# Performance work log

Measured on AMD Instinct MI355X. Metric: run time of the kernel, lower is better.

The kernel has to match this reference:

```python
import math
import jax, jax.numpy as jnp
import numpy as np

GRAIN = 300   # bilinear / grain dim (gpconv output channels)
PAD = 4       # explicit zero padding before each conv1d / conv2d
POOL = 40     # adaptive pool target (mf_model_pool_dim)

def conv1d_k2(x, w, b):
    # x: [B, L, Cin], w: [Cout, Cin, 2] -> [B, L-1, Cout]
    return (jnp.einsum('blc,oc->blo', x[:, :-1], w[:, :, 0])
            + jnp.einsum('blc,oc->blo', x[:, 1:], w[:, :, 1]) + b)

def kmax_last(x, k):
    # torch-style k-max pooling: top-k values along last axis, original order kept
    idx = jnp.sort(jax.lax.top_k(x, k)[1], axis=-1)
    return jnp.take_along_axis(x, idx, axis=-1)

def kmax_len(x, k):
    # k-max pooling over the length axis (axis=1) of [B, L, C]
    return jnp.swapaxes(kmax_last(jnp.swapaxes(x, 1, 2), k), 1, 2)

def adaptive_max_1d(x, out, axis):
    # torch AdaptiveMaxPool semantics along one axis; windows precomputed statically
    L = x.shape[axis]
    r = np.arange(out)
    starts = (r * L) // out
    ends = -((-(r + 1) * L) // out)
    maxw = int((ends - starts).max())
    off = starts[:, None] + np.arange(maxw)[None, :]
    mask = jnp.asarray(off < ends[:, None])
    idxs = np.minimum(off, L - 1)
    xm = jnp.moveaxis(x, axis, -1)
    g = jnp.where(mask, xm[..., idxs], -jnp.inf)
    return jnp.moveaxis(g.max(-1), -1, axis)

def conv2d_p4(x, w, b):
    y = jax.lax.conv_general_dilated(x, w, (1, 1), [(PAD, PAD), (PAD, PAD)],
                                     dimension_numbers=('NCHW', 'OIHW', 'NCHW'))
    return y + b[None, :, None, None]

def gp_tower(x, w1, b1, w2, b2, w3, b3, k1, k2):
    # multigranular conv tower: zero-pad(4) -> conv1d(k=2) -> tanh -> k-max pool
    g0 = kmax_last(x, GRAIN)                      # [B, L, 300]
    def block(z, w, b, k):
        z = jnp.pad(z, ((0, 0), (PAD, PAD), (0, 0)))
        return kmax_len(jnp.tanh(conv1d_k2(z, w, b)), k)
    p1 = block(x, w1, b1, k1)                     # [B, k1, 300]
    p2 = block(p1, w2, b2, k2)                    # [B, k2, 300]
    p3 = block(p2, w3, b3, 1)                     # [B, 1, 300]
    return jnp.concatenate([g0, p1, p2, p3], axis=1)

def _forward(query, pos_doc, neg_docs, qw1, qb1, qw2, qb2, qw3, qb3,
             dw1, db1, dw2, db2, dw3, db3, bw, bb,
             mw1, mb1, mw2, mb2, mw3, mb3, lw, lb):
    B, Lq, _ = query.shape
    S, _, Ld, _ = neg_docs.shape
    kq1, kq2 = max(4, math.ceil(2 * Lq / 3)), max(4, math.ceil(Lq / 3))
    kd1, kd2 = max(4, math.ceil(2 * Ld / 3)), max(4, math.ceil(Ld / 3))
    qg = gp_tower(query, qw1, qb1, qw2, qb2, qw3, qb3, kq1, kq2)   # [B, Nq, 300]
    docs = jnp.concatenate([pos_doc[None], neg_docs], 0).reshape((S + 1) * B, Ld, -1)
    dg = gp_tower(docs, dw1, db1, dw2, db2, dw3, db3, kd1, kd2)    # [(S+1)B, Nd, 300]
    Nq, Nd = qg.shape[1], dg.shape[1]
    dg = dg.reshape(S + 1, B, Nd, GRAIN)
    # batched bilinear matching + sigmoid (replaces the O(Nq*Nd) per-pair loop)
    qt = jnp.einsum('bqd,de->bqe', qg, bw)
    M = jax.nn.sigmoid(jnp.einsum('bqe,sbje->sbqj', qt, dg) + bb[0])
    M = M.reshape((S + 1) * B, Nq, Nd)
    x = adaptive_max_1d(adaptive_max_1d(M, POOL, 1), POOL, 2)[:, None]  # [N,1,40,40]
    for w, b in ((mw1, mb1), (mw2, mb2), (mw3, mb3)):
        x = jax.nn.sigmoid(conv2d_p4(x, w, b))
        x = adaptive_max_1d(adaptive_max_1d(x, POOL, 2), POOL, 3)
        x = x.max(axis=1, keepdims=True)          # k-max(k=1) over channels
    feat = x[:, 0]                                # [N, 40, 40]
    h = jax.nn.sigmoid(jnp.einsum('nij,j->ni', feat, lw[0]) + lb[0])
    s = jax.nn.sigmoid(h @ lw[0] + lb[0])
    return s.reshape(S + 1, B)                    # row 0 = pos-doc scores

def setup_inputs():
    ks = jax.random.split(jax.random.key(0), 26)
    def n(i, shape, s=0.05):
        return jax.random.normal(ks[i], shape, dtype=jnp.float32) * s
    return dict(
        query=jax.random.normal(ks[0], (16, 239, 1024), dtype=jnp.float32),
        pos_doc=jax.random.normal(ks[1], (16, 479, 1024), dtype=jnp.float32),
        neg_docs=jax.random.normal(ks[2], (4, 16, 479, 1024), dtype=jnp.float32),
        qw1=n(3, (300, 1024, 2)), qb1=n(4, (300,)),
        qw2=n(5, (300, 300, 2)), qb2=n(6, (300,)),
        qw3=n(7, (300, 300, 2)), qb3=n(8, (300,)),
        dw1=n(9, (300, 1024, 2)), db1=n(10, (300,)),
        dw2=n(11, (300, 300, 2)), db2=n(12, (300,)),
        dw3=n(13, (300, 300, 2)), db3=n(14, (300,)),
        bw=n(15, (300, 300)), bb=n(16, (1,)),
        mw1=n(17, (50, 1, 2, 2)), mb1=n(18, (50,)),
        mw2=n(19, (50, 1, 2, 2)), mb2=n(20, (50,)),
        mw3=n(21, (50, 1, 2, 2)), mb3=n(22, (50,)),
        lw=n(23, (1, 40)), lb=n(24, (1,)),
    )

def reference(query, pos_doc, neg_docs, qw1, qb1, qw2, qb2, qw3, qb3,
              dw1, db1, dw2, db2, dw3, db3, bw, bb,
              mw1, mb1, mw2, mb2, mw3, mb3, lw, lb):
    return _forward(query, pos_doc, neg_docs, qw1, qb1, qw2, qb2, qw3, qb3,
                    dw1, db1, dw2, db2, dw3, db3, bw, bb,
                    mw1, mb1, mw2, mb2, mw3, mb3, lw, lb)
```

## Files before the change

kernel.cpp:

```cpp
#include <hip/hip_runtime.h>
#include <hip/hip_bf16.h>
#include <math.h>

typedef unsigned long long ull;
typedef unsigned int uint;
typedef unsigned short ushort_t;

typedef short bf16x8 __attribute__((ext_vector_type(8)));
typedef float floatx4 __attribute__((ext_vector_type(4)));

__device__ inline ushort_t f2b(float f) {
    uint u = __float_as_uint(f);
    u = u + 0x7fffu + ((u >> 16) & 1u);
    return (ushort_t)(u >> 16);
}

__device__ inline uint kmap16(ushort_t u) {
    return (u & 0x8000u) ? (uint)((~u) & 0xFFFFu) : (uint)(u | 0x8000u);
}
__device__ inline ushort_t kinv16(uint k) {
    return (k & 0x8000u) ? (ushort_t)(k ^ 0x8000u) : (ushort_t)((~k) & 0xFFFFu);
}

__device__ inline void async_copy16(const void* g, void* l) {
    __builtin_amdgcn_global_load_lds(
        (const __attribute__((address_space(1))) void*)g,
        (__attribute__((address_space(3))) void*)l, 16, 0, 0);
}

__global__ void prep_w2_kernel(const float* __restrict__ w, ushort_t* __restrict__ Wb,
                               int C, int CP) {
    int CHn = CP / 32;
    int total = CHn * 2 * 20 * 512;
    for (int i = blockIdx.x * blockDim.x + threadIdx.x; i < total;
         i += gridDim.x * blockDim.x) {
        int e = i & 7;
        int lane = (i >> 3) & 63;
        int rest = i >> 9;
        int g = rest % 20;
        int tc = rest / 20;
        int t = tc & 1, c = tc >> 1;
        int o = g * 16 + (lane & 15);
        int ch = c * 32 + (lane >> 4) * 8 + e;
        float v = (o < 300 && ch < C) ? w[((size_t)o * C + ch) * 2 + t] : 0.f;
        Wb[i] = f2b(v);
    }
}

__global__ void prep_bw_kernel(const float* __restrict__ bw, ushort_t* __restrict__ bwb) {
    int i = blockIdx.x * 256 + threadIdx.x;
    if (i >= 320 * 320) return;
    int e = i / 320, d = i - e * 320;
    bwb[i] = (e < 300 && d < 300) ? f2b(bw[d * 300 + e]) : (ushort_t)0;
}

__global__ __launch_bounds__(256) void x_pad_bf16_kernel(
    const float* __restrict__ src, const float* __restrict__ src2, int split_n,
    long long s_nstr, int Lin, ushort_t* __restrict__ dst, int rows)
{
    int r = blockIdx.x, n = blockIdx.y;
    const float* sp = (split_n > 0 && n >= split_n)
                          ? src2 + (size_t)(n - split_n) * s_nstr
                          : src + (size_t)n * s_nstr;
    int g = r - 4;
    ushort_t* dp = dst + ((size_t)n * rows + r) * 1024;
    int c = threadIdx.x * 4;
    ushort4 o = {0, 0, 0, 0};
    if (g >= 0 && g < Lin) {
        float4 v = *(const float4*)&sp[(size_t)g * 1024 + c];
        o.x = f2b(v.x); o.y = f2b(v.y); o.z = f2b(v.z); o.w = f2b(v.w);
    }
    *(ushort4*)&dp[c] = o;
}

template <int CP>
__global__ __launch_bounds__(256, 2) void conv_lds_kernel(
    const ushort_t* __restrict__ xq, long long xq_nstr,
    const ushort_t* __restrict__ xd, long long xd_nstr,
    const ushort_t* __restrict__ Wq, const ushort_t* __restrict__ Wd,
    const float* __restrict__ bq, const float* __restrict__ bd,
    int Lout_q, int Lout_d, int mtiles_q,
    ushort_t* __restrict__ yt)
{
    constexpr int CH = CP / 32;
    constexpr int BUFB = 65 * 64;
    __shared__ ushort_t Abuf[3][65 * 32];

    int mt = blockIdx.x, n = blockIdx.y;
    bool isq = (n < 16);
    if (isq && mt >= mtiles_q) return;
    const ushort_t* x = isq ? xq + (size_t)n * xq_nstr
                            : xd + (size_t)(n - 16) * xd_nstr;
    const ushort_t* W = isq ? Wq : Wd;
    const float* bias = isq ? bq : bd;
    int Lout = isq ? Lout_q : Lout_d;
    int l0 = mt * 64;

    int tid = threadIdx.x, wid = tid >> 6, lane = tid & 63;
    int wn = wid * 80;
    int lrow = lane & 15, quad = lane >> 4;

    int srow = tid >> 2;
    int sslot = (tid & 3) ^ ((tid >> 3) & 3);
    const ushort_t* gMain = x + (size_t)(l0 + srow) * CP + sslot * 8;
    const ushort_t* gXtra = x + (size_t)(l0 + 64) * CP + wid * 8;

    const ushort_t* Bw = W + ((size_t)wid * 5) * 512 + lane * 8;

    int offA[2][4];
#pragma unroll
    for (int t = 0; t < 2; t++)
#pragma unroll
        for (int ms = 0; ms < 4; ms++) {
            int r = ms * 16 + lrow + t;
            offA[t][ms] = r * 64 + ((quad ^ ((r >> 1) & 3)) << 4);
        }

    floatx4 acc[4][5];
#pragma unroll
    for (int i = 0; i < 4; i++)
#pragma unroll
        for (int j = 0; j < 5; j++) acc[i][j] = (floatx4){0.f, 0.f, 0.f, 0.f};

    char* lds0 = (char*)&Abuf[0][0];

    auto STAGE = [&](int cc, int slot) {
        char* lb = lds0 + slot * BUFB;
        async_copy16(gMain + cc * 32, lb + wid * 1024);
        if (lane == 0) async_copy16(gXtra + cc * 32, lb + 4096 + wid * 16);
    };
    auto LOADB = [&](bf16x8 (&bf)[2][5], int cc) {
#pragma unroll
        for (int t = 0; t < 2; t++)
#pragma unroll
            for (int ns = 0; ns < 5; ns++)
                bf[t][ns] = *(const bf16x8*)(Bw + (size_t)((cc * 2 + t) * 20 + ns) * 512);
    };
    auto COMPUTE = [&](bf16x8 (&bf)[2][5], int rslot) {
        const char* ab = lds0 + rslot * BUFB;
        __builtin_amdgcn_s_setprio(1);
#pragma unroll
        for (int t = 0; t < 2; t++) {
            bf16x8 af[4];
#pragma unroll
            for (int ms = 0; ms < 4; ms++)
                af[ms] = *(const bf16x8*)(ab + offA[t][ms]);
#pragma unroll
            for (int ms = 0; ms < 4; ms++)
#pragma unroll
                for (int ns = 0; ns < 5; ns++)
                    acc[ms][ns] = __builtin_amdgcn_mfma_f32_16x16x32_bf16(
                        af[ms], bf[t][ns], acc[ms][ns], 0, 0, 0);
        }
        __builtin_amdgcn_s_setprio(0);
    };
    auto WAITBAR = [&]() {
        asm volatile("s_waitcnt vmcnt(10)" ::: "memory");
        __builtin_amdgcn_s_barrier();
        __builtin_amdgcn_sched_barrier(0);
    };

    bf16x8 bA[2][5], bB[2][5];

    STAGE(0, 0);
    LOADB(bA, 0);
    STAGE(1, 1);

    int sl = 0;
    for (int c = 0; c < CH; c += 2) {
        int rA = sl;
        int rB = rA + 1; if (rB == 3) rB = 0;
        int wA = rB + 1; if (wA == 3) wA = 0;
        int wB = rA;

        WAITBAR();
        LOADB(bB, c + 1);
        __builtin_amdgcn_sched_barrier(0x38F);
        if (c + 2 < CH) STAGE(c + 2, wA);
        COMPUTE(bA, rA);

        WAITBAR();
        if (c + 2 < CH) LOADB(bA, c + 2);
        __builtin_amdgcn_sched_barrier(0x38F);
        if (c + 3 < CH) STAGE(c + 3, wB);
        COMPUTE(bB, rB);

        sl = wA;
    }

    ushort_t* yp = yt + (size_t)n * 488 * 320;
#pragma unroll
    for (int ns = 0; ns < 5; ns++) {
        int o = wn + ns * 16 + lrow;
        if (o >= 300) continue;
        float bo = bias[o];
#pragma unroll
        for (int ms = 0; ms < 4; ms++)
#pragma unroll
            for (int r = 0; r < 4; r++) {
                int l = l0 + ms * 16 + quad * 4 + r;
                if (l < Lout)
                    yp[(size_t)l * 320 + o] = f2b(tanhf(acc[ms][ns][r] + bo));
            }
    }
}

template <int EPT>
__global__ __launch_bounds__(256) void topk16_kernel(
    const ushort_t* __restrict__ src, int CC,
    long long s_n, long long s_c, long long s_e,
    int L, int k,
    ushort_t* __restrict__ out1, long long o1_off, long long o1_n,
    long long o1_c, long long o1_e,
    ushort_t* __restrict__ out2, long long o2_off, long long o2_n,
    long long o2_c, long long o2_e)
{
    __shared__ uint sbuf[257];
    __shared__ uint wtot[4];
    __shared__ uint bsel[2];
    __shared__ uint wsum[4];

    int row = blockIdx.x;
    int n = row / CC, c = row - n * CC;
    const ushort_t* sp = src + (size_t)n * s_n + (size_t)c * s_c;

    int tid = threadIdx.x, lane = tid & 63, wid = tid >> 6;
    int base = tid * EPT;

    uint key[EPT];
    if (EPT == 4 && s_e == 1) {
        ushort4 v = *(const ushort4*)&sp[base];
        key[0] = kmap16(v.x); key[1] = kmap16(v.y);
        key[2] = kmap16(v.z); key[3] = kmap16(v.w);
    } else {
#pragma unroll
        for (int e = 0; e < EPT; e++) {
            int i = base + e;
            key[e] = (i < L) ? kmap16(sp[(size_t)i * s_e]) : 0u;
        }
    }

    uint pmask = 0, pval = 0, rem = (uint)k;
#pragma unroll
    for (int shift = 8; shift >= 0; shift -= 8) {
        sbuf[tid] = 0;
        __syncthreads();
#pragma unroll
        for (int e = 0; e < EPT; e++) {
            int i = base + e;
            if (i < L && (key[e] & pmask) == pval)
                atomicAdd(&sbuf[(key[e] >> shift) & 255], 1u);
        }
        __syncthreads();
        uint sfx = sbuf[tid];
#pragma unroll
        for (int off = 1; off < 64; off <<= 1) {
            uint u2 = __shfl_down(sfx, off);
            if (lane + off < 64) sfx += u2;
        }
        if (lane == 0) wtot[wid] = sfx;
        __syncthreads();
        uint hi = 0;
        for (int w = wid + 1; w < 4; w++) hi += wtot[w];
        sbuf[tid] = sfx + hi;
        if (tid == 0) sbuf[256] = 0;
        __syncthreads();
        uint cg = sbuf[tid], cgn = sbuf[tid + 1];
        if (cg >= rem && cgn < rem) { bsel[0] = (uint)tid; bsel[1] = rem - cgn; }
        __syncthreads();
        pval |= bsel[0] << shift;
        pmask |= 0xFFu << shift;
        rem = bsel[1];
        __syncthreads();
    }

    const uint T = pval;
    uint gtc = 0, eqc = 0;
#pragma unroll
    for (int e = 0; e < EPT; e++) {
        int i = base + e;
        if (i < L) {
            gtc += (key[e] > T) ? 1u : 0u;
            eqc += (key[e] == T) ? 1u : 0u;
        }
    }
    uint pack = (gtc << 16) | eqc;
    uint incl = pack;
#pragma unroll
    for (int off = 1; off < 64; off <<= 1) {
        uint u2 = __shfl_up(incl, off);
        if (lane >= off) incl += u2;
    }
    uint excl = incl - pack;
    if (lane == 63) wsum[wid] = incl;
    __syncthreads();
    uint badd = 0;
    for (int w = 0; w < wid; w++) badd += wsum[w];
    excl += badd;
    uint gt_before = excl >> 16, eq_before = excl & 0xffffu;

    ushort_t* dp1 = out1 + (size_t)o1_off + (size_t)n * o1_n + (size_t)c * o1_c;
    ushort_t* dp2 = out2 ? out2 + (size_t)o2_off + (size_t)n * o2_n + (size_t)c * o2_c
                         : (ushort_t*)0;
#pragma unroll
    for (int e = 0; e < EPT; e++) {
        int i = base + e;
        if (i >= L) break;
        uint kk = key[e];
        if (kk > T) {
            uint pos = gt_before + (eq_before < rem ? eq_before : rem);
            ushort_t v = kinv16(kk);
            dp1[(size_t)pos * o1_e] = v;
            if (dp2) dp2[(size_t)pos * o2_e] = v;
            gt_before++;
        } else if (kk == T) {
            if (eq_before < rem) {
                uint pos = gt_before + eq_before;
                ushort_t v = kinv16(kk);
                dp1[(size_t)pos * o1_e] = v;
                if (dp2) dp2[(size_t)pos * o2_e] = v;
            }
            eq_before++;
        }
    }
}

__global__ __launch_bounds__(256) void qt_mfma_kernel(
    const ushort_t* __restrict__ qgb, const ushort_t* __restrict__ bwb,
    ushort_t* __restrict__ qtb)
{
    int mt = blockIdx.x, b = blockIdx.y;
    int tid = threadIdx.x, wid = tid >> 6, lane = tid & 63;
    int wn = wid * 80, lrow = lane & 15, quad = lane >> 4;

    const ushort_t* A = qgb + ((size_t)b * 480 + mt * 48 + lrow) * 320 + quad * 8;
    const ushort_t* B = bwb + (size_t)(wn + lrow) * 320 + quad * 8;

    floatx4 acc[3][5];
#pragma unroll
    for (int i = 0; i < 3; i++)
#pragma unroll
        for (int j = 0; j < 5; j++) acc[i][j] = (floatx4){0.f, 0.f, 0.f, 0.f};

#pragma unroll 5
    for (int c0 = 0; c0 < 320; c0 += 32) {
        bf16x8 af[3], bfr[5];
#pragma unroll
        for (int ms = 0; ms < 3; ms++)
            af[ms] = *(const bf16x8*)&A[(size_t)(ms * 16) * 320 + c0];
#pragma unroll
        for (int ns = 0; ns < 5; ns++)
            bfr[ns] = *(const bf16x8*)&B[(size_t)(ns * 16) * 320 + c0];
#pragma unroll
        for (int ms = 0; ms < 3; ms++)
#pragma unroll
            for (int ns = 0; ns < 5; ns++)
                acc[ms][ns] = __builtin_amdgcn_mfma_f32_16x16x32_bf16(
                    af[ms], bfr[ns], acc[ms][ns], 0, 0, 0);
    }

    ushort_t* out = qtb + ((size_t)b * 480 + mt * 48) * 320;
#pragma unroll
    for (int ms = 0; ms < 3; ms++)
#pragma unroll
        for (int ns = 0; ns < 5; ns++)
#pragma unroll
            for (int r = 0; r < 4; r++)
                out[(size_t)(ms * 16 + quad * 4 + r) * 320 + wn + ns * 16 + lrow] =
                    f2b(acc[ms][ns][r]);
}

__global__ __launch_bounds__(256) void mpool_mfma_kernel(
    const ushort_t* __restrict__ qtb16, const ushort_t* __restrict__ dgb16,
    const float* __restrict__ bb, float* __restrict__ mp)
{
    __shared__ float pool[2 * 12 * 192];

    int jb = blockIdx.x;
    int qb = blockIdx.y;
    int n  = blockIdx.z;
    int b  = n & 15;

    int tid = threadIdx.x;
    int wid = tid >> 6, lane = tid & 63;
    int wm2 = wid >> 1;
    int wm = wm2 * 48, wn = (wid & 1) * 96;
    int lrow = lane & 15, quad = lane >> 4;

    const ushort_t* Abase = qtb16 + ((size_t)b * 480 + qb * 96 + wm) * 320 + quad * 8;
    const ushort_t* Bbase = dgb16 + ((size_t)n * 960 + jb * 192 + wn) * 320 + quad * 8;

    floatx4 acc[3][6];
#pragma unroll
    for (int i = 0; i < 3; i++)
#pragma unroll
        for (int j = 0; j < 6; j++) acc[i][j] = (floatx4){0.f, 0.f, 0.f, 0.f};

#pragma unroll 2
    for (int c0 = 0; c0 < 320; c0 += 32) {
        bf16x8 af[3], bfr[6];
#pragma unroll
        for (int mt = 0; mt < 3; mt++)
            af[mt] = *(const bf16x8*)&Abase[(size_t)(mt * 16 + lrow) * 320 + c0];
#pragma unroll
        for (int nt = 0; nt < 6; nt++)
            bfr[nt] = *(const bf16x8*)&Bbase[(size_t)(nt * 16 + lrow) * 320 + c0];
#pragma unroll
        for (int mt = 0; mt < 3; mt++)
#pragma unroll
            for (int nt = 0; nt < 6; nt++)
                acc[mt][nt] = __builtin_amdgcn_mfma_f32_16x16x32_bf16(
                    af[mt], bfr[nt], acc[mt][nt], 0, 0, 0);
    }

#pragma unroll
    for (int mt = 0; mt < 3; mt++) {
        int g = mt * 4 + quad;
#pragma unroll
        for (int nt = 0; nt < 6; nt++) {
            floatx4 a = acc[mt][nt];
            float rm = fmaxf(fmaxf(a[0], a[1]), fmaxf(a[2], a[3]));
            pool[(wm2 * 12 + g) * 192 + wn + nt * 16 + lrow] = rm;
        }
    }
    __syncthreads();

    if (tid < 64) {
        int qw = tid >> 3, jw = tid & 7;
        int slab = qw >> 2, w = qw & 3;
        float m = -INFINITY;
        const float* pp = &pool[(slab * 12 + w * 3) * 192 + jw * 24];
        for (int g = 0; g < 3; g++)
            for (int cc = 0; cc < 24; cc++)
                m = fmaxf(m, pp[g * 192 + cc]);
        float sig = 1.f / (1.f + expf(-(m + bb[0])));
        mp[(size_t)n * 1600 + (size_t)(qb * 8 + qw) * 40 + (jb * 8 + jw)] = sig;
    }
}

#define OCG 10
__global__ __launch_bounds__(256) void convblock_atomic_kernel(
    const float* __restrict__ X, const float* __restrict__ w,
    const float* __restrict__ bias, uint* __restrict__ Y)
{
    __shared__ float xp[48 * 48];
    __shared__ float ys[47 * 47];
    __shared__ float t1[40 * 47];
    __shared__ float outacc[1600];

    int n = blockIdx.x, t = threadIdx.x;
    int oc0 = blockIdx.y * OCG;
    const float* xn = X + (size_t)n * 1600;
    for (int i = t; i < 48 * 48; i += 256) {
        int r = i / 48, c = i - r * 48;
        int rr = r - 4, cc = c - 4;
        xp[i] = (rr >= 0 && rr < 40 && cc >= 0 && cc < 40) ? xn[rr * 40 + cc] : 0.f;
    }
    for (int i = t; i < 1600; i += 256) outacc[i] = 0.f;
    __syncthreads();

    for (int oc = oc0; oc < oc0 + OCG; oc++) {
        float w00 = w[oc * 4 + 0], w01 = w[oc * 4 + 1];
        float w10 = w[oc * 4 + 2], w11 = w[oc * 4 + 3];
        float bo = bias[oc];
        for (int i = t; i < 47 * 47; i += 256) {
            int r = i / 47, c = i - r * 47;
            float v = xp[r * 48 + c] * w00 + xp[r * 48 + c + 1] * w01
                    + xp[(r + 1) * 48 + c] * w10 + xp[(r + 1) * 48 + c + 1] * w11 + bo;
            ys[i] = 1.f / (1.f + expf(-v));
        }
        __syncthreads();
        for (int i = t; i < 40 * 47; i += 256) {
            int r = i / 47, c = i - r * 47;
            int s = (47 * r) / 40, e = (47 * (r + 1) + 39) / 40;
            float m = ys[s * 47 + c];
            for (int x = s + 1; x < e; x++) m = fmaxf(m, ys[x * 47 + c]);
            t1[i] = m;
        }
        __syncthreads();
        for (int i = t; i < 1600; i += 256) {
            int r = i / 40, c = i - r * 40;
            int s = (47 * c) / 40, e = (47 * (c + 1) + 39) / 40;
            float m = t1[r * 47 + s];
            for (int x = s + 1; x < e; x++) m = fmaxf(m, t1[r * 47 + x]);
            outacc[i] = fmaxf(outacc[i], m);
        }
        __syncthreads();
    }
    for (int i = t; i < 1600; i += 256)
        atomicMax(&Y[(size_t)n * 1600 + i], __float_as_uint(outacc[i]));
}

__global__ __launch_bounds__(64) void head_kernel(
    const float* __restrict__ feat, const float* __restrict__ lw,
    const float* __restrict__ lb, float* __restrict__ out)
{
    __shared__ float hs[40];
    int n = blockIdx.x, t = threadIdx.x;
    const float* f = feat + (size_t)n * 1600;
    if (t < 40) {
        float a = 0.f;
        for (int j = 0; j < 40; j++) a += f[t * 40 + j] * lw[j];
        hs[t] = 1.f / (1.f + expf(-(a + lb[0])));
    }
    __syncthreads();
    if (t == 0) {
        float a = 0.f;
        for (int i = 0; i < 40; i++) a += hs[i] * lw[i];
        out[n] = 1.f / (1.f + expf(-(a + lb[0])));
    }
}

extern "C" void kernel_launch(void* const* d_in, const int* in_sizes, int n_in,
                              void* d_out, int out_size, void* d_ws, size_t ws_size,
                              hipStream_t stream) {
    const float* query    = (const float*)d_in[0];
    const float* pos_doc  = (const float*)d_in[1];
    const float* neg_docs = (const float*)d_in[2];
    const float* qw1 = (const float*)d_in[3];  const float* qb1 = (const float*)d_in[4];
    const float* qw2 = (const float*)d_in[5];  const float* qb2 = (const float*)d_in[6];
    const float* qw3 = (const float*)d_in[7];  const float* qb3 = (const float*)d_in[8];
    const float* dw1 = (const float*)d_in[9];  const float* db1 = (const float*)d_in[10];
    const float* dw2 = (const float*)d_in[11]; const float* db2 = (const float*)d_in[12];
    const float* dw3 = (const float*)d_in[13]; const float* db3 = (const float*)d_in[14];
    const float* bw  = (const float*)d_in[15]; const float* bb  = (const float*)d_in[16];
    const float* mw1 = (const float*)d_in[17]; const float* mb1 = (const float*)d_in[18];
    const float* mw2 = (const float*)d_in[19]; const float* mb2 = (const float*)d_in[20];
    const float* mw3 = (const float*)d_in[21]; const float* mb3 = (const float*)d_in[22];
    const float* lw  = (const float*)d_in[23]; const float* lb  = (const float*)d_in[24];

    float* ws = (float*)d_ws;
    ushort_t* qw1b  = (ushort_t*)(ws + 0);
    ushort_t* qw2b  = (ushort_t*)(ws + 327680);
    ushort_t* qw3b  = (ushort_t*)(ws + 430080);
    ushort_t* dw1b  = (ushort_t*)(ws + 532480);
    ushort_t* dw2b  = (ushort_t*)(ws + 860160);
    ushort_t* dw3b  = (ushort_t*)(ws + 962560);
    ushort_t* bwb   = (ushort_t*)(ws + 1064960);
    ushort_t* qgb16 = (ushort_t*)(ws + 1116160);
    ushort_t* dgb16 = (ushort_t*)(ws + 2344960);
    ushort_t* yt    = (ushort_t*)(ws + 14632960);
    ushort_t* qxb   = (ushort_t*)(ws + 22128640);
    ushort_t* p1q   = (ushort_t*)(ws + 22128640);
    ushort_t* p2q   = (ushort_t*)(ws + 22640640);
    ushort_t* dxb   = (ushort_t*)(ws + 24291328);
    ushort_t* p1d   = (ushort_t*)(ws + 24291328);
    ushort_t* p2d   = (ushort_t*)(ws + 28899328);
    ushort_t* qtb16 = (ushort_t*)(ws + 31459328);
    float*    mp    = ws + 32688128;
    float*    ya    = ws + 32816128;
    float*    yb    = ws + 32944128;
    float*    yc    = ws + 33072128;

    prep_w2_kernel<<<1280, 256, 0, stream>>>(qw1, qw1b, 1024, 1024);
    prep_w2_kernel<<<400, 256, 0, stream>>>(qw2, qw2b, 300, 320);
    prep_w2_kernel<<<400, 256, 0, stream>>>(qw3, qw3b, 300, 320);
    prep_w2_kernel<<<1280, 256, 0, stream>>>(dw1, dw1b, 1024, 1024);
    prep_w2_kernel<<<400, 256, 0, stream>>>(dw2, dw2b, 300, 320);
    prep_w2_kernel<<<400, 256, 0, stream>>>(dw3, dw3b, 300, 320);
    prep_bw_kernel<<<400, 256, 0, stream>>>(bw, bwb);

    {
        dim3 g(264, 16);
        x_pad_bf16_kernel<<<g, 256, 0, stream>>>(query, nullptr, 0,
                                                 239LL * 1024, 239, qxb, 264);
    }
    {
        dim3 g(520, 80);
        x_pad_bf16_kernel<<<g, 256, 0, stream>>>(pos_doc, neg_docs, 16,
                                                 479LL * 1024, 479, dxb, 520);
    }

    topk16_kernel<4><<<16 * 239, 256, 0, stream>>>(
        qxb + 4 * 1024, 239, 264LL * 1024, 1024, 1, 1024, 300,
        qgb16, 0, 480LL * 320, 320, 1,
        nullptr, 0, 0, 0, 0);
    topk16_kernel<4><<<80 * 479, 256, 0, stream>>>(
        dxb + 4 * 1024, 479, 520LL * 1024, 1024, 1, 1024, 300,
        dgb16, 0, 960LL * 320, 320, 1,
        nullptr, 0, 0, 0, 0);

    {
        dim3 g(8, 96);
        conv_lds_kernel<1024><<<g, 256, 0, stream>>>(
            qxb, 264LL * 1024, dxb, 520LL * 1024,
            qw1b, dw1b, qb1, db1, 246, 486, 4, yt);
    }

    hipMemsetAsync(p1q, 0, 16 * 200 * 320 * 2, stream);
    hipMemsetAsync(p2q, 0, 16 * 104 * 320 * 2, stream);
    hipMemsetAsync(p1d, 0, (size_t)80 * 360 * 320 * 2, stream);
    hipMemsetAsync(p2d, 0, (size_t)80 * 200 * 320 * 2, stream);
    hipMemsetAsync(ya, 0, 80 * 1600 * 4, stream);
    hipMemsetAsync(yb, 0, 80 * 1600 * 4, stream);
    hipMemsetAsync(yc, 0, 80 * 1600 * 4, stream);

    topk16_kernel<1><<<16 * 300, 256, 0, stream>>>(
        yt, 300, 488LL * 320, 1, 320, 246, 160,
        qgb16, 239LL * 320, 480LL * 320, 1, 320,
        p1q, 4LL * 320, 200LL * 320, 1, 320);
    topk16_kernel<2><<<80 * 300, 256, 0, stream>>>(
        yt + (size_t)16 * 488 * 320, 300, 488LL * 320, 1, 320, 486, 320,
        dgb16, 479LL * 320, 960LL * 320, 1, 320,
        p1d, 4LL * 320, 360LL * 320, 1, 320);

    {
        dim3 g(6, 96);
        conv_lds_kernel<320><<<g, 256, 0, stream>>>(
            p1q, 200LL * 320, p1d, 360LL * 320,
            qw2b, dw2b, qb2, db2, 167, 327, 3, yt);
    }

    topk16_kernel<1><<<16 * 300, 256, 0, stream>>>(
        yt, 300, 488LL * 320, 1, 320, 167, 80,
        qgb16, 399LL * 320, 480LL * 320, 1, 320,
        p2q, 4LL * 320, 104LL * 320, 1, 320);
    topk16_kernel<2><<<80 * 300, 256, 0, stream>>>(
        yt + (size_t)16 * 488 * 320, 300, 488LL * 320, 1, 320, 327, 160,
        dgb16, 799LL * 320, 960LL * 320, 1, 320,
        p2d, 4LL * 320, 200LL * 320, 1, 320);

    {
        dim3 g(3, 96);
        conv_lds_kernel<320><<<g, 256, 0, stream>>>(
            p2q, 104LL * 320, p2d, 200LL * 320,
            qw3b, dw3b, qb3, db3, 87, 167, 2, yt);
    }

    topk16_kernel<1><<<16 * 300, 256, 0, stream>>>(
        yt, 300, 488LL * 320, 1, 320, 87, 1,
        qgb16, 479LL * 320, 480LL * 320, 1, 320,
        nullptr, 0, 0, 0, 0);
    topk16_kernel<1><<<80 * 300, 256, 0, stream>>>(
        yt + (size_t)16 * 488 * 320, 300, 488LL * 320, 1, 320, 167, 1,
        dgb16, 959LL * 320, 960LL * 320, 1, 320,
        nullptr, 0, 0, 0, 0);

    {
        dim3 g(10, 16);
        qt_mfma_kernel<<<g, 256, 0, stream>>>(qgb16, bwb, qtb16);
    }
    {
        dim3 g(5, 5, 80);
        mpool_mfma_kernel<<<g, 256, 0, stream>>>(qtb16, dgb16, bb, mp);
    }

    {
        dim3 g(80, 5);
        convblock_atomic_kernel<<<g, 256, 0, stream>>>(mp, mw1, mb1, (uint*)ya);
        convblock_atomic_kernel<<<g, 256, 0, stream>>>(ya, mw2, mb2, (uint*)yb);
        convblock_atomic_kernel<<<g, 256, 0, stream>>>(yb, mw3, mb3, (uint*)yc);
    }
    head_kernel<<<80, 64, 0, stream>>>(yc, lw, lb, (float*)d_out);
}
```

Measured before the change: 1.244 ms.

## Transpose conv output to channel-major and batch 32 channels per top-k block

Result: faster. 1.132 ms (-9.0%).

```diff
diff --git a/kernel.cpp b/kernel.cpp
--- a/kernel.cpp
+++ b/kernel.cpp
@@ -188,20 +188,29 @@
         sl = wA;
     }
 
-    ushort_t* yp = yt + (size_t)n * 488 * 320;
+    ushort_t* yp = yt + (size_t)n * (320 * 488);
 #pragma unroll
     for (int ns = 0; ns < 5; ns++) {
         int o = wn + ns * 16 + lrow;
         if (o >= 300) continue;
         float bo = bias[o];
-#pragma unroll
-        for (int ms = 0; ms < 4; ms++)
-#pragma unroll
-            for (int r = 0; r < 4; r++) {
-                int l = l0 + ms * 16 + quad * 4 + r;
-                if (l < Lout)
-                    yp[(size_t)l * 320 + o] = f2b(tanhf(acc[ms][ns][r] + bo));
+        ushort_t* orow = yp + (size_t)o * 488;
+#pragma unroll
+        for (int ms = 0; ms < 4; ms++) {
+            int l = l0 + ms * 16 + quad * 4;
+            if (l + 3 < Lout) {
+                ushort4 v;
+                v.x = f2b(tanhf(acc[ms][ns][0] + bo));
+                v.y = f2b(tanhf(acc[ms][ns][1] + bo));
+                v.z = f2b(tanhf(acc[ms][ns][2] + bo));
+                v.w = f2b(tanhf(acc[ms][ns][3] + bo));
+                *(ushort4*)&orow[l] = v;
+            } else {
+#pragma unroll
+                for (int r = 0; r < 4; r++)
+                    if (l + r < Lout) orow[l + r] = f2b(tanhf(acc[ms][ns][r] + bo));
             }
+        }
     }
 }
 
@@ -322,6 +331,130 @@
             }
             eq_before++;
         }
+    }
+}
+
+__global__ __launch_bounds__(256) void topk_cols_kernel(
+    const ushort_t* __restrict__ yt2,
+    int Lq, int Ld, int kq, int kd,
+    ushort_t* __restrict__ qg, int qoff,
+    ushort_t* __restrict__ dg, int doff,
+    ushort_t* __restrict__ pq, long long pq_nstr,
+    ushort_t* __restrict__ pd, long long pd_nstr)
+{
+    __shared__ __align__(16) ushort_t xin[32][488];
+    __shared__ __align__(16) uint hist[32 * 257];
+    ushort_t* otile = (ushort_t*)hist;
+
+    int cg = blockIdx.x, n = blockIdx.y;
+    int c0 = cg * 32;
+    bool isq = (n < 16);
+    int L = isq ? Lq : Ld;
+    int k = isq ? kq : kd;
+    int nd = isq ? n : n - 16;
+    int tid = threadIdx.x;
+
+    const ushort_t* src = yt2 + (size_t)n * (320 * 488) + (size_t)c0 * 488;
+    for (int i = tid; i < 32 * 61; i += 256) {
+        int j = i / 61, s = i - j * 61;
+        *(uint4*)&xin[j][s * 8] = *(const uint4*)&src[(size_t)j * 488 + s * 8];
+    }
+    __syncthreads();
+
+    int g = tid >> 3, r = tid & 7;
+    uint* hg = &hist[g * 257];
+    bool cval = (c0 + g) < 300;
+    int S = (L + 7) >> 3;
+    int llo = r * S, lhi = llo + S;
+    if (lhi > L) lhi = L;
+    if (llo > L) llo = L;
+
+    uint rem = (uint)k;
+    uint bsel = 0;
+    uint Tt = 0;
+
+#pragma unroll
+    for (int round = 0; round < 2; round++) {
+        for (int t = r; t < 256; t += 8) hg[t] = 0;
+        for (int l = llo; l < lhi; l++) {
+            uint key = cval ? kmap16(xin[g][l]) : 0x8000u;
+            if (round == 0)
+                atomicAdd(&hg[key >> 8], 1u);
+            else if ((key >> 8) == bsel)
+                atomicAdd(&hg[key & 255u], 1u);
+        }
+        uint hv[32];
+        uint Sr = 0;
+        int b0 = r * 32;
+#pragma unroll
+        for (int t = 0; t < 32; t++) { hv[t] = hg[b0 + t]; Sr += hv[t]; }
+        uint suf = Sr;
+#pragma unroll
+        for (int off = 1; off < 8; off <<= 1) {
+            uint u = __shfl_down(suf, off);
+            if (r + off < 8) suf += u;
+        }
+        uint acc = suf - Sr;
+        uint found = 0;
+#pragma unroll
+        for (int t = 31; t >= 0; t--) {
+            uint h = hv[t];
+            if (!found && acc < rem && acc + h >= rem)
+                found = ((uint)(b0 + t) << 16) | (rem - acc);
+            acc += h;
+        }
+#pragma unroll
+        for (int off = 1; off < 8; off <<= 1) found |= __shfl_xor(found, off);
+        if (round == 0) {
+            bsel = found >> 16;
+            rem = found & 0xffffu;
+        } else {
+            Tt = (bsel << 8) | (found >> 16);
+            rem = found & 0xffffu;
+        }
+    }
+
+    uint gtc = 0, eqc = 0;
+    for (int l = llo; l < lhi; l++) {
+        uint key = cval ? kmap16(xin[g][l]) : 0x8000u;
+        gtc += (key > Tt) ? 1u : 0u;
+        eqc += (key == Tt) ? 1u : 0u;
+    }
+    uint pack = (gtc << 16) | eqc, incl = pack;
+#pragma unroll
+    for (int off = 1; off < 8; off <<= 1) {
+        uint u = __shfl_up(incl, off);
+        if (r >= off) incl += u;
+    }
+    uint excl = incl - pack;
+    uint gt_b = excl >> 16, eq_b = excl & 0xffffu;
+
+    __syncthreads();
+
+    for (int l = llo; l < lhi; l++) {
+        uint key = cval ? kmap16(xin[g][l]) : 0x8000u;
+        if (key > Tt) {
+            uint pos = gt_b + (eq_b < rem ? eq_b : rem);
+            otile[pos * 32 + g] = kinv16(key);
+            gt_b++;
+        } else if (key == Tt) {
+            if (eq_b < rem) otile[(gt_b + eq_b) * 32 + g] = kinv16(key);
+            eq_b++;
+        }
+    }
+    __syncthreads();
+
+    ushort_t* d1 = isq ? qg + ((size_t)nd * 480 + qoff) * 320 + c0
+                       : dg + ((size_t)nd * 960 + doff) * 320 + c0;
+    ushort_t* d2 = 0;
+    if (isq) { if (pq) d2 = pq + (size_t)nd * pq_nstr + 4 * 320 + c0; }
+    else     { if (pd) d2 = pd + (size_t)nd * pd_nstr + 4 * 320 + c0; }
+
+    for (int i = tid; i < k * 8; i += 256) {
+        int p = i >> 3, s = i & 7;
+        ushort4 v = *(ushort4*)&otile[p * 32 + s * 4];
+        *(ushort4*)&d1[(size_t)p * 320 + s * 4] = v;
+        if (d2) *(ushort4*)&d2[(size_t)p * 320 + s * 4] = v;
     }
 }
 
@@ -595,14 +728,13 @@
     hipMemsetAsync(yb, 0, 80 * 1600 * 4, stream);
     hipMemsetAsync(yc, 0, 80 * 1600 * 4, stream);
 
-    topk16_kernel<1><<<16 * 300, 256, 0, stream>>>(
-        yt, 300, 488LL * 320, 1, 320, 246, 160,
-        qgb16, 239LL * 320, 480LL * 320, 1, 320,
-        p1q, 4LL * 320, 200LL * 320, 1, 320);
-    topk16_kernel<2><<<80 * 300, 256, 0, stream>>>(
-        yt + (size_t)16 * 488 * 320, 300, 488LL * 320, 1, 320, 486, 320,
-        dgb16, 479LL * 320, 960LL * 320, 1, 320,
-        p1d, 4LL * 320, 360LL * 320, 1, 320);
+    {
+        dim3 g(10, 96);
+        topk_cols_kernel<<<g, 256, 0, stream>>>(
+            yt, 246, 486, 160, 320,
+            qgb16, 239, dgb16, 479,
+            p1q, 200LL * 320, p1d, 360LL * 320);
+    }
 
     {
         dim3 g(6, 96);
@@ -611,14 +743,13 @@
             qw2b, dw2b, qb2, db2, 167, 327, 3, yt);
     }
 
-    topk16_kernel<1><<<16 * 300, 256, 0, stream>>>(
-        yt, 300, 488LL * 320, 1, 320, 167, 80,
-        qgb16, 399LL * 320, 480LL * 320, 1, 320,
-        p2q, 4LL * 320, 104LL * 320, 1, 320);
-    topk16_kernel<2><<<80 * 300, 256, 0, stream>>>(
-        yt + (size_t)16 * 488 * 320, 300, 488LL * 320, 1, 320, 327, 160,
-        dgb16, 799LL * 320, 960LL * 320, 1, 320,
-        p2d, 4LL * 320, 200LL * 320, 1, 320);
+    {
+        dim3 g(10, 96);
+        topk_cols_kernel<<<g, 256, 0, stream>>>(
+            yt, 167, 327, 80, 160,
+            qgb16, 399, dgb16, 799,
+            p2q, 104LL * 320, p2d, 200LL * 320);
+    }
 
     {
         dim3 g(3, 96);
@@ -627,14 +758,13 @@
             qw3b, dw3b, qb3, db3, 87, 167, 2, yt);
     }
 
-    topk16_kernel<1><<<16 * 300, 256, 0, stream>>>(
-        yt, 300, 488LL * 320, 1, 320, 87, 1,
-        qgb16, 479LL * 320, 480LL * 320, 1, 320,
-        nullptr, 0, 0, 0, 0);
-    topk16_kernel<1><<<80 * 300, 256, 0, stream>>>(
-        yt + (size_t)16 * 488 * 320, 300, 488LL * 320, 1, 320, 167, 1,
-        dgb16, 959LL * 320, 960LL * 320, 1, 320,
-        nullptr, 0, 0, 0, 0);
+    {
+        dim3 g(10, 96);
+        topk_cols_kernel<<<g, 256, 0, stream>>>(
+            yt, 87, 167, 1, 1,
+            qgb16, 479, dgb16, 959,
+            nullptr, 0, nullptr, 0);
+    }
 
     {
         dim3 g(10, 16);
```
